# Performance work log

Hardware: AMD Instinct MI355X
Metric: run time of the kernel (lower is better)

## Reference

```python
import jax, jax.numpy as jnp
import numpy as np
from jax import lax

EPS = 1e-5
CLIP = 1.3  # Hardtanh(-1.3, 1.3)


def hardtanh(v):
    return jnp.clip(v, -CLIP, CLIP)


def binarize(v):
    # sign() forward with straight-through (identity) gradient, as in BCNN BinarizeF
    return v + lax.stop_gradient(jnp.sign(v) - v)


def bc_conv(x, w):
    # binarized conv: binarize both activations and weights, 3x3, stride 1, pad 1
    return lax.conv_general_dilated(
        binarize(x), binarize(w),
        window_strides=(1, 1), padding=((1, 1), (1, 1)),
        dimension_numbers=("NCHW", "OIHW", "NCHW"))


def batchnorm(v, gamma, beta):
    # batch statistics over (N, H, W), per-channel affine (DC_Bn4 variant)
    mean = jnp.mean(v, axis=(0, 2, 3), keepdims=True)
    var = jnp.var(v, axis=(0, 2, 3), keepdims=True)
    inv = lax.rsqrt(var + EPS)
    return (v - mean) * inv * gamma[None, :, None, None] + beta[None, :, None, None]


def setup_inputs() -> dict:
    key = jax.random.key(0)
    k_x, k_w1, k_w2 = jax.random.split(key, 3)
    C = 32
    x = jax.random.normal(k_x, (16, C, 224, 224), dtype=jnp.float32)
    w1 = jax.random.normal(k_w1, (C, C, 3, 3), dtype=jnp.float32) * 0.1
    w2 = jax.random.normal(k_w2, (C, C, 3, 3), dtype=jnp.float32) * 0.1
    g1 = jnp.ones((C,), jnp.float32); b1 = jnp.zeros((C,), jnp.float32)
    g2 = jnp.ones((C,), jnp.float32); b2 = jnp.zeros((C,), jnp.float32)
    return {"x": x, "w1": w1, "g1": g1, "b1": b1, "w2": w2, "g2": g2, "b2": b2}


def reference(x, w1, g1, b1, w2, g2, b2):
    y = batchnorm(bc_conv(hardtanh(x), w1), g1, b1)
    y = batchnorm(bc_conv(hardtanh(y), w2), g2, b2)
    return x + y
```

## Files before the change

### kernel.cpp

```cpp
#include <hip/hip_runtime.h>
#include <stdint.h>

#define NB 16
#define CC 32
#define HH 224
#define WW 224
#define HWP (HH*WW)
#define NHWP (NB*HWP)
#define PW 226
#define PSZ (PW*PW)

#define OFF_S1   0u
#define OFF_S2   3268864u
#define OFF_WP1  6537728u
#define OFF_WP2  6538880u
#define OFF_SQ1  6540032u
#define OFF_SQ2  6544128u
#define OFF_SUM1 6548224u
#define OFF_SUM2 6550272u
#define OFF_BF1  6552320u
#define OFF_BF2  6561536u
#define OFF_CACHE 6572032u
#define CACHE_BYTES 51380224u

typedef int v4i    __attribute__((ext_vector_type(4)));
typedef int i32x16 __attribute__((ext_vector_type(16)));

__global__ void __launch_bounds__(256) k_setup(const uint32_t* __restrict__ w1,
                                               const uint32_t* __restrict__ w2,
                                               char* __restrict__ ws) {
    int t = blockIdx.x * 256 + threadIdx.x;
    if (t < 576) {
        const uint32_t* w = (t < 288) ? w1 : w2;
        uint32_t* o = (uint32_t*)(ws + ((t < 288) ? OFF_WP1 : OFF_WP2));
        int idx = (t < 288) ? t : t - 288;
        int oc = idx / 9, k = idx - oc * 9;
        uint32_t word = 0;
        for (int i = 0; i < 32; ++i)
            word |= (w[(oc * 32 + i) * 9 + k] >> 31) << i;
        o[idx] = word;
    } else if (t < 3648) {
        ((uint32_t*)(ws + OFF_SQ1))[t - 576] = 0u;
    } else if (t >= 4096 && t < 32896) {
        int b = t - 4096;
        uint32_t* buf = (uint32_t*)(ws + ((b < 14400) ? OFF_S1 : OFF_S2));
        int bb = (b < 14400) ? b : b - 14400;
        int n = bb / 900;
        int e = bb - n * 900;
        int row, col;
        if (e < 226)      { row = 0;   col = e; }
        else if (e < 452) { row = 225; col = e - 226; }
        else { int k = e - 452; row = 1 + (k >> 1); col = (k & 1) ? 225 : 0; }
        buf[(size_t)n * PSZ + row * PW + col] = 0u;
    } else if (t >= 32896 && t < 34048) {
        int idx = t - 32896;
        int layer = idx / 576, rem = idx - layer * 576;
        int tap = rem / 64, lane = rem - tap * 64;
        int oc = lane & 31, kb = (lane >> 5) * 16;
        const uint32_t* w = layer ? w2 : w1;
        uint32_t dw[4];
        #pragma unroll
        for (int d = 0; d < 4; ++d) {
            uint32_t v = 0x01010101u;
            #pragma unroll
            for (int b = 0; b < 4; ++b) {
                uint32_t sgn = w[(oc * 32 + kb + 4 * d + b) * 9 + tap] >> 31;
                v ^= (0xFEu * sgn) << (8 * b);
            }
            dw[d] = v;
        }
        uint4* o = (uint4*)(ws + (layer ? OFF_BF2 : OFF_BF1));
        o[tap * 64 + lane] = make_uint4(dw[0], dw[1], dw[2], dw[3]);
    }
}

__global__ void __launch_bounds__(256) k_packx(const uint32_t* __restrict__ x,
                                               uint32_t* __restrict__ sp) {
    int t = blockIdx.x * 256 + threadIdx.x;
    int n = t / (HWP / 4);
    int rem4 = t - n * (HWP / 4);
    int px0 = rem4 * 4;
    int r = px0 / WW;
    int cw0 = px0 - r * WW;
    const uint32_t* xp = x + (size_t)n * CC * HWP + px0;
    uint32_t w0 = 0, w1 = 0, w2 = 0, w3 = 0;
    #pragma unroll
    for (int c = 0; c < 32; ++c) {
        uint4 v = *reinterpret_cast<const uint4*>(xp + (size_t)c * HWP);
        w0 |= (v.x >> 31) << c;
        w1 |= (v.y >> 31) << c;
        w2 |= (v.z >> 31) << c;
        w3 |= (v.w >> 31) << c;
    }
    uint32_t* op = sp + (size_t)n * PSZ + (r + 1) * PW + (cw0 + 1);
    op[0] = w0; op[1] = w1; op[2] = w2; op[3] = w3;
}

#define ASTRIDE 48
#define AROW (226*ASTRIDE)

__device__ __forceinline__ uint32_t spread4(uint32_t nib) {
    uint32_t s = (nib & 1u) | ((nib & 2u) << 7) | ((nib & 4u) << 14) | ((nib & 8u) << 21);
    return 0x01010101u ^ (s * 0xFEu);
}

__device__ __forceinline__ i32x16 conv_mfma(const uint32_t* __restrict__ sp,
                                            const v4i* __restrict__ bfp,
                                            int n, int r, char* At) {
    for (int s = threadIdx.x; s < 3 * 226; s += 448) {
        int dr = s / 226, cc = s - dr * 226;
        int srow = r - 1 + dr, scol = cc - 1;
        uint32_t d8[8];
        if (srow < 0 || srow >= HH || scol < 0 || scol >= WW) {
            #pragma unroll
            for (int i = 0; i < 8; ++i) d8[i] = 0u;
        } else {
            uint32_t w = sp[(size_t)n * PSZ + (srow + 1) * PW + (scol + 1)];
            #pragma unroll
            for (int i = 0; i < 8; ++i) d8[i] = spread4((w >> (4 * i)) & 0xFu);
        }
        uint32_t* p = (uint32_t*)(At + s * ASTRIDE);
        *(uint4*)(p)     = make_uint4(d8[0], d8[1], d8[2], d8[3]);
        *(uint4*)(p + 4) = make_uint4(d8[4], d8[5], d8[6], d8[7]);
    }

    int l = threadIdx.x & 63;
    v4i bf[9];
    #pragma unroll
    for (int t = 0; t < 9; ++t) bf[t] = bfp[t * 64 + l];
    __syncthreads();

    int wavebase = (threadIdx.x >> 6) * 32;
    int base = (wavebase + (l & 31)) * ASTRIDE + (l >> 5) * 16;

    i32x16 acc = {0,0,0,0,0,0,0,0,0,0,0,0,0,0,0,0};
    #pragma unroll
    for (int dh = 0; dh < 3; ++dh) {
        #pragma unroll
        for (int dw = 0; dw < 3; ++dw) {
            v4i a = *reinterpret_cast<const v4i*>(At + base + dh * AROW + dw * ASTRIDE);
            acc = __builtin_amdgcn_mfma_i32_32x32x32_i8(a, bf[dh * 3 + dw], acc, 0, 0, 0);
        }
    }
    return acc;
}

__global__ void __launch_bounds__(448) k_stats(const uint32_t* __restrict__ sp,
                                               const v4i* __restrict__ bfp,
                                               int* __restrict__ g_sum,
                                               unsigned long long* __restrict__ g_sq,
                                               int16_t* __restrict__ cache) {
    __shared__ __align__(16) char At[3 * 226 * ASTRIDE];
    __shared__ int ls[7][32], lq[7][32];

    int n = blockIdx.x / HH, r = blockIdx.x - n * HH;
    i32x16 acc = conv_mfma(sp, bfp, n, r, At);

    int l = threadIdx.x & 63;
    if (cache) {
        int oc = l & 31, hi = l >> 5;
        int wavebase = (threadIdx.x >> 6) * 32;
        int16_t* cp = cache + ((size_t)n * CC + oc) * HWP + (size_t)r * WW;
        #pragma unroll
        for (int g = 0; g < 4; ++g) {
            int px0 = wavebase + 8 * g + 4 * hi;
            short4 sv;
            sv.x = (short)acc[4 * g + 0];
            sv.y = (short)acc[4 * g + 1];
            sv.z = (short)acc[4 * g + 2];
            sv.w = (short)acc[4 * g + 3];
            *reinterpret_cast<short4*>(cp + px0) = sv;
        }
    }

    int s = 0, q = 0;
    #pragma unroll
    for (int g = 0; g < 16; ++g) { int c = acc[g]; s += c; q += c * c; }
    s += __shfl_xor(s, 32, 64);
    q += __shfl_xor(q, 32, 64);
    int wid = threadIdx.x >> 6;
    if (l < 32) { ls[wid][l] = s; lq[wid][l] = q; }
    __syncthreads();
    if (threadIdx.x < 32) {
        int S = 0, Q = 0;
        #pragma unroll
        for (int w = 0; w < 7; ++w) { S += ls[w][threadIdx.x]; Q += lq[w][threadIdx.x]; }
        int bin = blockIdx.x & 15;
        atomicAdd(&g_sum[bin * 32 + threadIdx.x], S);
        atomicAdd(&g_sq[bin * 32 + threadIdx.x], (unsigned long long)(long long)Q);
    }
}

__device__ __forceinline__ void build_affine16(const int* __restrict__ g_sum,
                                               const unsigned long long* __restrict__ g_sq,
                                               const float* __restrict__ gamma,
                                               const float* __restrict__ beta,
                                               float* aL, float* dL) {
    if (threadIdx.x < 32) {
        int c = threadIdx.x;
        int Si = 0; unsigned long long Qu = 0;
        #pragma unroll
        for (int b = 0; b < 16; ++b) { Si += g_sum[b * 32 + c]; Qu += g_sq[b * 32 + c]; }
        double M = (double)NHWP;
        double mean = (double)Si / M;
        double ex2 = (double)(long long)Qu / M;
        double var = ex2 - mean * mean;
        double inv = 1.0 / sqrt(var + 1e-5);
        double aa = inv * (double)gamma[c];
        aL[c] = (float)aa;
        dL[c] = (float)((double)beta[c] - aa * mean);
    }
}

__global__ void __launch_bounds__(256) k_signc(const int16_t* __restrict__ cache,
                                               const int* __restrict__ g_sum,
                                               const unsigned long long* __restrict__ g_sq,
                                               const float* __restrict__ gamma,
                                               const float* __restrict__ beta,
                                               uint32_t* __restrict__ op) {
    __shared__ float aL[32], dL[32];
    build_affine16(g_sum, g_sq, gamma, beta, aL, dL);
    __syncthreads();

    int t = blockIdx.x * 256 + threadIdx.x;
    int n = t / (HWP / 4);
    int rem4 = t - n * (HWP / 4);
    int px0 = rem4 * 4;
    int r = px0 / WW;
    int cw0 = px0 - r * WW;
    const int16_t* cp = cache + (size_t)n * CC * HWP + px0;
    uint32_t w0 = 0, w1 = 0, w2 = 0, w3 = 0;
    #pragma unroll
    for (int c = 0; c < 32; ++c) {
        short4 v = *reinterpret_cast<const short4*>(cp + (size_t)c * HWP);
        float a = aL[c], d = dL[c];
        w0 |= (__float_as_uint(fmaf(a, (float)v.x, d)) >> 31) << c;
        w1 |= (__float_as_uint(fmaf(a, (float)v.y, d)) >> 31) << c;
        w2 |= (__float_as_uint(fmaf(a, (float)v.z, d)) >> 31) << c;
        w3 |= (__float_as_uint(fmaf(a, (float)v.w, d)) >> 31) << c;
    }
    uint32_t* o = op + (size_t)n * PSZ + (r + 1) * PW + (cw0 + 1);
    o[0] = w0; o[1] = w1; o[2] = w2; o[3] = w3;
}

__global__ void __launch_bounds__(256) k_resc(const int16_t* __restrict__ cache,
                                              const int* __restrict__ g_sum,
                                              const unsigned long long* __restrict__ g_sq,
                                              const float* __restrict__ gamma,
                                              const float* __restrict__ beta,
                                              const float* __restrict__ x,
                                              float* __restrict__ out) {
    __shared__ float aL[32], dL[32];
    build_affine16(g_sum, g_sq, gamma, beta, aL, dL);
    __syncthreads();

    int t = blockIdx.x * 256 + threadIdx.x;
    int n = t / (HWP / 4);
    int rem4 = t - n * (HWP / 4);
    int px0 = rem4 * 4;
    const int16_t* cp = cache + (size_t)n * CC * HWP + px0;
    const float* xp = x + (size_t)n * CC * HWP + px0;
    float* op = out + (size_t)n * CC * HWP + px0;
    #pragma unroll
    for (int c = 0; c < 32; ++c) {
        short4 v = *reinterpret_cast<const short4*>(cp + (size_t)c * HWP);
        float a = aL[c], d = dL[c];
        float4 xv = *reinterpret_cast<const float4*>(xp + (size_t)c * HWP);
        float4 ov;
        ov.x = xv.x + fmaf(a, (float)v.x, d);
        ov.y = xv.y + fmaf(a, (float)v.y, d);
        ov.z = xv.z + fmaf(a, (float)v.z, d);
        ov.w = xv.w + fmaf(a, (float)v.w, d);
        *reinterpret_cast<float4*>(op + (size_t)c * HWP) = ov;
    }
}

__global__ void __launch_bounds__(448) k_sign_f(const uint32_t* __restrict__ sp,
                                                const v4i* __restrict__ bfp,
                                                const int* __restrict__ g_sum,
                                                const unsigned long long* __restrict__ g_sq,
                                                const float* __restrict__ gamma,
                                                const float* __restrict__ beta,
                                                uint32_t* __restrict__ op) {
    __shared__ __align__(16) char At[3 * 226 * ASTRIDE];
    __shared__ float aL[32], dL[32];
    build_affine16(g_sum, g_sq, gamma, beta, aL, dL);

    int n = blockIdx.x / HH, r = blockIdx.x - n * HH;
    i32x16 acc = conv_mfma(sp, bfp, n, r, At);

    int l = threadIdx.x & 63;
    int wavebase = (threadIdx.x >> 6) * 32;
    float a = aL[l & 31], d = dL[l & 31];
    uint32_t* orow = op + (size_t)n * PSZ + (r + 1) * PW + 1 + wavebase;
    #pragma unroll
    for (int g = 0; g < 16; ++g) {
        float y = fmaf(a, (float)acc[g], d);
        unsigned long long b = __ballot((__float_as_uint(y) >> 31) != 0u);
        if (l == 0) {
            int pxr = (g & 3) + 8 * (g >> 2);
            orow[pxr]     = (uint32_t)b;
            orow[pxr + 4] = (uint32_t)(b >> 32);
        }
    }
}

__global__ void __launch_bounds__(448) k_res_f(const uint32_t* __restrict__ sp,
                                               const v4i* __restrict__ bfp,
                                               const int* __restrict__ g_sum,
                                               const unsigned long long* __restrict__ g_sq,
                                               const float* __restrict__ gamma,
                                               const float* __restrict__ beta,
                                               const float* __restrict__ x,
                                               float* __restrict__ out) {
    __shared__ __align__(16) char At[3 * 226 * ASTRIDE];
    __shared__ float aL[32], dL[32];
    build_affine16(g_sum, g_sq, gamma, beta, aL, dL);

    int n = blockIdx.x / HH, r = blockIdx.x - n * HH;
    i32x16 acc = conv_mfma(sp, bfp, n, r, At);

    int l = threadIdx.x & 63;
    int oc = l & 31, hi = l >> 5;
    int wavebase = (threadIdx.x >> 6) * 32;
    float a = aL[oc], d = dL[oc];
    size_t rowoff = (size_t)n * CC * HWP + (size_t)oc * HWP + (size_t)r * WW;
    #pragma unroll
    for (int g = 0; g < 4; ++g) {
        int px0 = wavebase + 8 * g + 4 * hi;
        float4 xv = *reinterpret_cast<const float4*>(x + rowoff + px0);
        float4 ov;
        ov.x = xv.x + fmaf(a, (float)acc[4 * g + 0], d);
        ov.y = xv.y + fmaf(a, (float)acc[4 * g + 1], d);
        ov.z = xv.z + fmaf(a, (float)acc[4 * g + 2], d);
        ov.w = xv.w + fmaf(a, (float)acc[4 * g + 3], d);
        *reinterpret_cast<float4*>(out + rowoff + px0) = ov;
    }
}

extern "C" void kernel_launch(void* const* d_in, const int* in_sizes, int n_in,
                              void* d_out, int out_size, void* d_ws, size_t ws_size,
                              hipStream_t stream) {
    const float* x  = (const float*)d_in[0];
    const float* w1 = (const float*)d_in[1];
    const float* g1 = (const float*)d_in[2];
    const float* b1 = (const float*)d_in[3];
    const float* w2 = (const float*)d_in[4];
    const float* g2 = (const float*)d_in[5];
    const float* b2 = (const float*)d_in[6];
    float* out = (float*)d_out;

    char* ws = (char*)d_ws;
    uint32_t* s1  = (uint32_t*)(ws + OFF_S1);
    uint32_t* s2  = (uint32_t*)(ws + OFF_S2);
    const v4i* bf1 = (const v4i*)(ws + OFF_BF1);
    const v4i* bf2 = (const v4i*)(ws + OFF_BF2);
    unsigned long long* sq1 = (unsigned long long*)(ws + OFF_SQ1);
    unsigned long long* sq2 = (unsigned long long*)(ws + OFF_SQ2);
    int* sum1 = (int*)(ws + OFF_SUM1);
    int* sum2 = (int*)(ws + OFF_SUM2);
    bool useCache = ws_size >= (size_t)OFF_CACHE + (size_t)CACHE_BYTES;
    int16_t* cache = useCache ? (int16_t*)(ws + OFF_CACHE) : (int16_t*)nullptr;

    k_setup<<<134, 256, 0, stream>>>((const uint32_t*)w1, (const uint32_t*)w2, ws);
    k_packx<<<784, 256, 0, stream>>>((const uint32_t*)x, s1);
    k_stats<<<3584, 448, 0, stream>>>(s1, bf1, sum1, sq1, cache);
    if (useCache) {
        k_signc<<<784, 256, 0, stream>>>(cache, sum1, sq1, g1, b1, s2);
        k_stats<<<3584, 448, 0, stream>>>(s2, bf2, sum2, sq2, cache);
        k_resc <<<784, 256, 0, stream>>>(cache, sum2, sq2, g2, b2, x, out);
    } else {
        k_sign_f<<<3584, 448, 0, stream>>>(s1, bf1, sum1, sq1, g1, b1, s2);
        k_stats<<<3584, 448, 0, stream>>>(s2, bf2, sum2, sq2, cache);
        k_res_f<<<3584, 448, 0, stream>>>(s2, bf2, sum2, sq2, g2, b2, x, out);
    }
}
```

Baseline: 291.2 us.

## Store int16 conv cache channel-last (NHWC) and remap sign/residual kernels per pixel

Changes the int16 conv-output cache from NCHW to NHWC so each pixel's 32 channels are contiguous. The sign-pack and residual kernels now assign one thread per pixel, reading 64 contiguous bytes with int4 loads, and the grids grow fourfold. The cache writes in k_stats become 2-byte scattered stores with a 64-byte stride, and the residual kernel now does scalar float loads and stores per channel instead of float4.

```diff
diff --git a/kernel.cpp b/kernel.cpp
--- a/kernel.cpp
+++ b/kernel.cpp
@@ -160,16 +160,14 @@
     if (cache) {
         int oc = l & 31, hi = l >> 5;
         int wavebase = (threadIdx.x >> 6) * 32;
-        int16_t* cp = cache + ((size_t)n * CC + oc) * HWP + (size_t)r * WW;
+        int16_t* cp = cache + (((size_t)n * HH + r) * WW) * CC + oc;
         #pragma unroll
         for (int g = 0; g < 4; ++g) {
-            int px0 = wavebase + 8 * g + 4 * hi;
-            short4 sv;
-            sv.x = (short)acc[4 * g + 0];
-            sv.y = (short)acc[4 * g + 1];
-            sv.z = (short)acc[4 * g + 2];
-            sv.w = (short)acc[4 * g + 3];
-            *reinterpret_cast<short4*>(cp + px0) = sv;
+            #pragma unroll
+            for (int j = 0; j < 4; ++j) {
+                int px = wavebase + 8 * g + 4 * hi + j;
+                cp[(size_t)px * CC] = (int16_t)acc[4 * g + j];
+            }
         }
     }
 
@@ -223,24 +221,26 @@
     __syncthreads();
 
     int t = blockIdx.x * 256 + threadIdx.x;
-    int n = t / (HWP / 4);
-    int rem4 = t - n * (HWP / 4);
-    int px0 = rem4 * 4;
-    int r = px0 / WW;
-    int cw0 = px0 - r * WW;
-    const int16_t* cp = cache + (size_t)n * CC * HWP + px0;
-    uint32_t w0 = 0, w1 = 0, w2 = 0, w3 = 0;
-    #pragma unroll
-    for (int c = 0; c < 32; ++c) {
-        short4 v = *reinterpret_cast<const short4*>(cp + (size_t)c * HWP);
-        float a = aL[c], d = dL[c];
-        w0 |= (__float_as_uint(fmaf(a, (float)v.x, d)) >> 31) << c;
-        w1 |= (__float_as_uint(fmaf(a, (float)v.y, d)) >> 31) << c;
-        w2 |= (__float_as_uint(fmaf(a, (float)v.z, d)) >> 31) << c;
-        w3 |= (__float_as_uint(fmaf(a, (float)v.w, d)) >> 31) << c;
-    }
-    uint32_t* o = op + (size_t)n * PSZ + (r + 1) * PW + (cw0 + 1);
-    o[0] = w0; o[1] = w1; o[2] = w2; o[3] = w3;
+    int n = t / HWP;
+    int px = t - n * HWP;
+    int r = px / WW, cw = px - r * WW;
+    const int4* cp = (const int4*)(cache + (size_t)t * CC);
+    uint32_t word = 0;
+    #pragma unroll
+    for (int k = 0; k < 4; ++k) {
+        int4 qv = cp[k];
+        int c0 = k * 8;
+        int vals[8] = { (int)(short)(qv.x & 0xFFFF), (int)(short)(qv.x >> 16),
+                        (int)(short)(qv.y & 0xFFFF), (int)(short)(qv.y >> 16),
+                        (int)(short)(qv.z & 0xFFFF), (int)(short)(qv.z >> 16),
+                        (int)(short)(qv.w & 0xFFFF), (int)(short)(qv.w >> 16) };
+        #pragma unroll
+        for (int j = 0; j < 8; ++j) {
+            float y = fmaf(aL[c0 + j], (float)vals[j], dL[c0 + j]);
+            word |= (__float_as_uint(y) >> 31) << (c0 + j);
+        }
+    }
+    op[(size_t)n * PSZ + (r + 1) * PW + (cw + 1)] = word;
 }
 
 __global__ void __launch_bounds__(256) k_resc(const int16_t* __restrict__ cache,
@@ -255,23 +255,24 @@
     __syncthreads();
 
     int t = blockIdx.x * 256 + threadIdx.x;
-    int n = t / (HWP / 4);
-    int rem4 = t - n * (HWP / 4);
-    int px0 = rem4 * 4;
-    const int16_t* cp = cache + (size_t)n * CC * HWP + px0;
-    const float* xp = x + (size_t)n * CC * HWP + px0;
-    float* op = out + (size_t)n * CC * HWP + px0;
-    #pragma unroll
-    for (int c = 0; c < 32; ++c) {
-        short4 v = *reinterpret_cast<const short4*>(cp + (size_t)c * HWP);
-        float a = aL[c], d = dL[c];
-        float4 xv = *reinterpret_cast<const float4*>(xp + (size_t)c * HWP);
-        float4 ov;
-        ov.x = xv.x + fmaf(a, (float)v.x, d);
-        ov.y = xv.y + fmaf(a, (float)v.y, d);
-        ov.z = xv.z + fmaf(a, (float)v.z, d);
-        ov.w = xv.w + fmaf(a, (float)v.w, d);
-        *reinterpret_cast<float4*>(op + (size_t)c * HWP) = ov;
+    int n = t / HWP;
+    int px = t - n * HWP;
+    const int4* cp = (const int4*)(cache + (size_t)t * CC);
+    const float* xp = x + (size_t)n * CC * HWP + px;
+    float* op = out + (size_t)n * CC * HWP + px;
+    #pragma unroll
+    for (int k = 0; k < 4; ++k) {
+        int4 qv = cp[k];
+        int c0 = k * 8;
+        int vals[8] = { (int)(short)(qv.x & 0xFFFF), (int)(short)(qv.x >> 16),
+                        (int)(short)(qv.y & 0xFFFF), (int)(short)(qv.y >> 16),
+                        (int)(short)(qv.z & 0xFFFF), (int)(short)(qv.z >> 16),
+                        (int)(short)(qv.w & 0xFFFF), (int)(short)(qv.w >> 16) };
+        #pragma unroll
+        for (int j = 0; j < 8; ++j) {
+            int c = c0 + j;
+            op[(size_t)c * HWP] = xp[(size_t)c * HWP] + fmaf(aL[c], (float)vals[j], dL[c]);
+        }
     }
 }
 
@@ -366,9 +367,9 @@
     k_packx<<<784, 256, 0, stream>>>((const uint32_t*)x, s1);
     k_stats<<<3584, 448, 0, stream>>>(s1, bf1, sum1, sq1, cache);
     if (useCache) {
-        k_signc<<<784, 256, 0, stream>>>(cache, sum1, sq1, g1, b1, s2);
+        k_signc<<<3136, 256, 0, stream>>>(cache, sum1, sq1, g1, b1, s2);
         k_stats<<<3584, 448, 0, stream>>>(s2, bf2, sum2, sq2, cache);
-        k_resc <<<784, 256, 0, stream>>>(cache, sum2, sq2, g2, b2, x, out);
+        k_resc <<<3136, 256, 0, stream>>>(cache, sum2, sq2, g2, b2, x, out);
     } else {
         k_sign_f<<<3584, 448, 0, stream>>>(s1, bf1, sum1, sq1, g1, b1, s2);
         k_stats<<<3584, 448, 0, stream>>>(s2, bf2, sum2, sq2, cache);
```

After: 278.3 us. 1.05x faster.
